# Optimization experiments

Hardware: AMD Instinct MI355X
Metric: run time of the kernel (lower is better)

## Reference

```python
import jax, jax.numpy as jnp
import numpy as np

BBOX_STD_DEV = jnp.array([0.1, 0.1, 0.2, 0.2], dtype=jnp.float32)
MIN_CONF = 0.15          # hardcoded in source (tf.where(probs >= 0.15))
NMS_THR = 0.3            # config.DETECTION_NMS_THRESHOLD
MAX_INST = 100           # config.DETECTION_MAX_INSTANCES
B, N = 8, 2048


def apply_box_deltas(boxes, deltas):
    # boxes: [N,4] (y1,x1,y2,x2); deltas: [N,4] (dy,dx,log dh,log dw)
    h = boxes[:, 2] - boxes[:, 0]
    w = boxes[:, 3] - boxes[:, 1]
    cy = boxes[:, 0] + 0.5 * h + deltas[:, 0] * h
    cx = boxes[:, 1] + 0.5 * w + deltas[:, 1] * w
    h = h * jnp.exp(deltas[:, 2])
    w = w * jnp.exp(deltas[:, 3])
    y1 = cy - 0.5 * h
    x1 = cx - 0.5 * w
    return jnp.stack([y1, x1, y1 + h, x1 + w], axis=1)


def clip_boxes(boxes, window):
    wy1, wx1, wy2, wx2 = window[0], window[1], window[2], window[3]
    y1 = jnp.clip(boxes[:, 0], wy1, wy2)
    x1 = jnp.clip(boxes[:, 1], wx1, wx2)
    y2 = jnp.clip(boxes[:, 2], wy1, wy2)
    x2 = jnp.clip(boxes[:, 3], wx1, wx2)
    return jnp.stack([y1, x1, y2, x2], axis=1)


def pairwise_iou(boxes):
    # boxes: [N,4] -> iou: [N,N]
    y1, x1, y2, x2 = boxes[:, 0], boxes[:, 1], boxes[:, 2], boxes[:, 3]
    area = (y2 - y1) * (x2 - x1)
    iy1 = jnp.maximum(y1[:, None], y1[None, :])
    ix1 = jnp.maximum(x1[:, None], x1[None, :])
    iy2 = jnp.minimum(y2[:, None], y2[None, :])
    ix2 = jnp.minimum(x2[:, None], x2[None, :])
    inter = jnp.maximum(iy2 - iy1, 0.0) * jnp.maximum(ix2 - ix1, 0.0)
    union = area[:, None] + area[None, :] - inter
    return inter / (union + 1e-8)


def refine_one(rois_i, probs_i, deltas_i, window_i):
    scores = probs_i[:, 0]
    boxes = clip_boxes(apply_box_deltas(rois_i, deltas_i * BBOX_STD_DEV), window_i)
    valid = scores >= MIN_CONF  # confidence filter (mask instead of gather)

    # sort by score descending; greedy NMS over sorted order
    order = jnp.argsort(-scores)
    sb, ss, sv = boxes[order], scores[order], valid[order]
    iou = pairwise_iou(sb)  # [N,N]
    idx = jnp.arange(N)

    def step(kept, xs):
        i, row, v = xs
        suppressed = jnp.any(kept & (idx < i) & (row > NMS_THR))
        return kept.at[i].set(v & ~suppressed), None

    kept, _ = jax.lax.scan(step, jnp.zeros((N,), dtype=bool), (idx, iou, sv))

    # top-k kept by score (already sorted desc, so top_k over masked scores)
    masked = jnp.where(kept, ss, -jnp.inf)
    _, top_i = jax.lax.top_k(masked, MAX_INST)
    ok = kept[top_i]
    det = jnp.concatenate([sb[top_i], ss[top_i][:, None]], axis=1)  # [MAX_INST,5]
    return jnp.where(ok[:, None], det, 0.0)  # zero-pad slots past num kept


def setup_inputs() -> dict:
    key = jax.random.key(0)
    k1, k2, k3 = jax.random.split(key, 3)
    # well-formed normalized rois: y1<y2, x1<x2
    yy = jnp.sort(jax.random.uniform(k1, (B, N, 2)), axis=-1)
    xx = jnp.sort(jax.random.uniform(jax.random.fold_in(k1, 1), (B, N, 2)), axis=-1)
    rois = jnp.stack([yy[..., 0], xx[..., 0], yy[..., 1], xx[..., 1]], axis=-1)
    bbox_scores = jax.random.uniform(k2, (B, N, 1), dtype=jnp.float32)
    deltas = jax.random.normal(k3, (B, N, 4), dtype=jnp.float32) * 0.1
    window = jnp.tile(jnp.array([[0.02, 0.02, 0.98, 0.98]], dtype=jnp.float32), (B, 1))
    return {"rois": rois, "bbox_scores": bbox_scores, "deltas": deltas, "window": window}


def reference(rois, bbox_scores, deltas, window):
    # -> [B, MAX_INST, 5] (y1,x1,y2,x2,score), normalized coords, zero padded
    return jax.vmap(refine_one)(rois, bbox_scores, deltas, window)
```

## Files before the change

kernel.cpp:

```cpp
#include <hip/hip_runtime.h>
#include <math.h>

#define NBOX 2048
#define NBATCH 8
#define MAX_INST 100
#define MIN_CONF 0.15f
#define NMS_THR 0.3f
#define BLOCK 512
#define NWAVE 8

typedef unsigned long long ull;

__device__ inline float4 decode_box(float4 r, float4 d,
                                    float wy1, float wx1, float wy2, float wx2) {
    float h  = __fsub_rn(r.z, r.x);
    float w  = __fsub_rn(r.w, r.y);
    float dy = __fmul_rn(d.x, 0.1f);
    float dx = __fmul_rn(d.y, 0.1f);
    float dh = __fmul_rn(d.z, 0.2f);
    float dw = __fmul_rn(d.w, 0.2f);
    float cy = __fadd_rn(__fadd_rn(r.x, __fmul_rn(0.5f, h)), __fmul_rn(dy, h));
    float cx = __fadd_rn(__fadd_rn(r.y, __fmul_rn(0.5f, w)), __fmul_rn(dx, w));
    float h2 = __fmul_rn(h, expf(dh));
    float w2 = __fmul_rn(w, expf(dw));
    float y1 = __fsub_rn(cy, __fmul_rn(0.5f, h2));
    float x1 = __fsub_rn(cx, __fmul_rn(0.5f, w2));
    float y2 = __fadd_rn(y1, h2);
    float x2 = __fadd_rn(x1, w2);
    float4 b;
    b.x = fminf(fmaxf(y1, wy1), wy2);
    b.y = fminf(fmaxf(x1, wx1), wx2);
    b.z = fminf(fmaxf(y2, wy1), wy2);
    b.w = fminf(fmaxf(x2, wx1), wx2);
    return b;
}

__device__ inline float iou_pair(float4 a, float4 b) {
    float areaA = __fmul_rn(__fsub_rn(a.z, a.x), __fsub_rn(a.w, a.y));
    float areaB = __fmul_rn(__fsub_rn(b.z, b.x), __fsub_rn(b.w, b.y));
    float iy1 = fmaxf(a.x, b.x);
    float ix1 = fmaxf(a.y, b.y);
    float iy2 = fminf(a.z, b.z);
    float ix2 = fminf(a.w, b.w);
    float ih = fmaxf(__fsub_rn(iy2, iy1), 0.0f);
    float iw = fmaxf(__fsub_rn(ix2, ix1), 0.0f);
    float inter = __fmul_rn(ih, iw);
    float uni = __fadd_rn(__fsub_rn(__fadd_rn(areaA, areaB), inter), 1e-8f);
    return __fdiv_rn(inter, uni);
}

__device__ inline ull shfl_xor64(ull x, int d) {
    unsigned lo = (unsigned)x, hi = (unsigned)(x >> 32);
    lo = __shfl_xor(lo, d);
    hi = __shfl_xor(hi, d);
    return ((ull)hi << 32) | lo;
}

__device__ inline void cmpsel(ull& a, ull& b, bool takeMinA) {
    ull mn = a < b ? a : b;
    ull mx = a < b ? b : a;
    a = takeMinA ? mn : mx;
    b = takeMinA ? mx : mn;
}

__global__ __launch_bounds__(BLOCK)
void detect_refine_kernel(const float* __restrict__ rois,
                          const float* __restrict__ scores_in,
                          const float* __restrict__ deltas,
                          const float* __restrict__ window,
                          float* __restrict__ out) {
    const int b    = blockIdx.x;
    const int tid  = threadIdx.x;
    const int lane = tid & 63;
    const int wid  = tid >> 6;

    __shared__ ull    keys[NBOX];
    __shared__ float4 sboxes[NBOX];
    __shared__ float  sscores[NBOX];
    __shared__ ull    dead8[NWAVE];
    __shared__ float4 s_keptbox[MAX_INST];
    __shared__ float  s_keptscore[MAX_INST];
    __shared__ int    s_m;

    const float wy1 = window[b * 4 + 0];
    const float wx1 = window[b * 4 + 1];
    const float wy2 = window[b * 4 + 2];
    const float wx2 = window[b * 4 + 3];

    float* outb = out + (size_t)b * MAX_INST * 5;

    for (int e = tid; e < NBOX; e += BLOCK) {
        float4 r = ((const float4*)rois)[b * NBOX + e];
        float4 d = ((const float4*)deltas)[b * NBOX + e];
        float  s = scores_in[b * NBOX + e];
        sboxes[e]  = decode_box(r, d, wy1, wx1, wy2, wx2);
        sscores[e] = s;
    }

    const int e0 = tid * 4;
    ull v[4];
    {
        float4 sc = ((const float4*)(scores_in + (size_t)b * NBOX))[tid];
        float s4[4] = {sc.x, sc.y, sc.z, sc.w};
#pragma unroll
        for (int s = 0; s < 4; ++s) {
            unsigned u = __float_as_uint(s4[s]);
            u = (u & 0x80000000u) ? ~u : (u | 0x80000000u);
            v[s] = ((ull)(~u) << 32) | (unsigned)(e0 + s);
        }
    }

    for (unsigned k = 2; k <= NBOX; k <<= 1) {
        if (k >= 512) {
#pragma unroll
            for (int s = 0; s < 4; ++s) keys[e0 + s] = v[s];
            __syncthreads();
            for (unsigned j = k >> 1; j >= 256; j >>= 1) {
                for (int t = tid; t < NBOX / 2; t += BLOCK) {
                    int i = 2 * t - (t & (j - 1));
                    int p = i | j;
                    bool up = ((i & k) == 0);
                    ull a = keys[i], c = keys[p];
                    bool sw = up ? (a > c) : (a < c);
                    if (sw) { keys[i] = c; keys[p] = a; }
                }
                __syncthreads();
            }
#pragma unroll
            for (int s = 0; s < 4; ++s) v[s] = keys[e0 + s];
        }
        unsigned jstart = ((k >> 1) > 128u) ? 128u : (k >> 1);
        for (unsigned j = jstart; j >= 4; j >>= 1) {
            int d = (int)(j >> 2);
#pragma unroll
            for (int s = 0; s < 4; ++s) {
                ull p = shfl_xor64(v[s], d);
                int e = e0 + s;
                bool takeMin = (((e & j) == 0) == ((e & k) == 0));
                v[s] = takeMin ? (v[s] < p ? v[s] : p) : (v[s] > p ? v[s] : p);
            }
        }
        if (k >= 4) {
            bool up = ((e0 & k) == 0);
            cmpsel(v[0], v[2], up);
            cmpsel(v[1], v[3], up);
        }
        {
            bool upA = ((e0 & k) == 0);
            bool upB = (((e0 + 2) & k) == 0);
            cmpsel(v[0], v[1], upA);
            cmpsel(v[2], v[3], upB);
        }
    }
#pragma unroll
    for (int s = 0; s < 4; ++s) keys[e0 + s] = v[s];
    __syncthreads();

    int count = 0;
    for (int base = 0; base < NBOX && count < MAX_INST; base += 64) {
        int    oi = (int)(keys[base + lane] & 0xFFFFFFFFull);
        float4 bj = sboxes[oi];
        float  sj = sscores[oi];

        bool deadp = (sj < MIN_CONF);
        for (int k = wid; k < count; k += NWAVE)
            deadp |= (iou_pair(s_keptbox[k], bj) > NMS_THR);
        ull bal = __ballot(deadp);
        if (lane == 0) dead8[wid] = bal;
        __syncthreads();

        if (wid == 0) {
            ull dead = dead8[0];
#pragma unroll
            for (int w2 = 1; w2 < NWAVE; ++w2) dead |= dead8[w2];
            ull alive = ~dead;
            int m = 0;
            const int maxm = MAX_INST - count;
            while (alive && m < maxm) {
                int i = __builtin_ctzll(alive);
                float4 kb;
                kb.x = __shfl(bj.x, i);
                kb.y = __shfl(bj.y, i);
                kb.z = __shfl(bj.z, i);
                kb.w = __shfl(bj.w, i);
                float ks = __shfl(sj, i);
                if (lane == 0) {
                    s_keptbox[count + m]   = kb;
                    s_keptscore[count + m] = ks;
                }
                ++m;
                ull sup = __ballot(iou_pair(kb, bj) > NMS_THR);
                alive &= ~sup;
                alive &= ~(1ull << i);
            }
            if (lane == 0) s_m = m;
        }
        __syncthreads();
        count += s_m;
    }

    for (int i = tid; i < MAX_INST * 5; i += BLOCK) {
        int r = i / 5, c = i % 5;
        float vout = 0.0f;
        if (r < count) {
            float4 bb = s_keptbox[r];
            vout = (c == 0) ? bb.x
                 : (c == 1) ? bb.y
                 : (c == 2) ? bb.z
                 : (c == 3) ? bb.w
                 :            s_keptscore[r];
        }
        outb[i] = vout;
    }
}

extern "C" void kernel_launch(void* const* d_in, const int* in_sizes, int n_in,
                              void* d_out, int out_size, void* d_ws, size_t ws_size,
                              hipStream_t stream) {
    const float* rois    = (const float*)d_in[0];
    const float* scores  = (const float*)d_in[1];
    const float* deltas  = (const float*)d_in[2];
    const float* window  = (const float*)d_in[3];
    float* out = (float*)d_out;
    detect_refine_kernel<<<NBATCH, BLOCK, 0, stream>>>(rois, scores, deltas, window, out);
}
```

Before: 47.05 us.

## Split into decode, sort and NMS kernels with 128-wide NMS chunks

```diff
diff --git a/kernel.cpp b/kernel.cpp
--- a/kernel.cpp
+++ b/kernel.cpp
@@ -6,8 +6,8 @@
 #define MAX_INST 100
 #define MIN_CONF 0.15f
 #define NMS_THR 0.3f
-#define BLOCK 512
-#define NWAVE 8
+#define SBLOCK 512
+#define NBLOCK 1024
 
 typedef unsigned long long ull;
 
@@ -63,40 +63,23 @@
     b = takeMinA ? mx : mn;
 }
 
-__global__ __launch_bounds__(BLOCK)
-void detect_refine_kernel(const float* __restrict__ rois,
-                          const float* __restrict__ scores_in,
-                          const float* __restrict__ deltas,
-                          const float* __restrict__ window,
-                          float* __restrict__ out) {
-    const int b    = blockIdx.x;
-    const int tid  = threadIdx.x;
-    const int lane = tid & 63;
-    const int wid  = tid >> 6;
-
-    __shared__ ull    keys[NBOX];
-    __shared__ float4 sboxes[NBOX];
-    __shared__ float  sscores[NBOX];
-    __shared__ ull    dead8[NWAVE];
-    __shared__ float4 s_keptbox[MAX_INST];
-    __shared__ float  s_keptscore[MAX_INST];
-    __shared__ int    s_m;
-
-    const float wy1 = window[b * 4 + 0];
-    const float wx1 = window[b * 4 + 1];
-    const float wy2 = window[b * 4 + 2];
-    const float wx2 = window[b * 4 + 3];
-
-    float* outb = out + (size_t)b * MAX_INST * 5;
-
-    for (int e = tid; e < NBOX; e += BLOCK) {
-        float4 r = ((const float4*)rois)[b * NBOX + e];
-        float4 d = ((const float4*)deltas)[b * NBOX + e];
-        float  s = scores_in[b * NBOX + e];
-        sboxes[e]  = decode_box(r, d, wy1, wx1, wy2, wx2);
-        sscores[e] = s;
-    }
-
+__global__ __launch_bounds__(256)
+void k_decode(const float* __restrict__ rois,
+              const float* __restrict__ deltas,
+              const float* __restrict__ window,
+              float4* __restrict__ wsbox) {
+    int g = blockIdx.x * 256 + threadIdx.x;
+    int b = g >> 11;
+    float4 r = ((const float4*)rois)[g];
+    float4 d = ((const float4*)deltas)[g];
+    wsbox[g] = decode_box(r, d, window[b * 4 + 0], window[b * 4 + 1],
+                          window[b * 4 + 2], window[b * 4 + 3]);
+}
+
+__global__ __launch_bounds__(SBLOCK)
+void k_sort(const float* __restrict__ scores_in, ull* __restrict__ wskeys) {
+    __shared__ ull keys[NBOX];
+    const int b = blockIdx.x, tid = threadIdx.x;
     const int e0 = tid * 4;
     ull v[4];
     {
@@ -109,14 +92,13 @@
             v[s] = ((ull)(~u) << 32) | (unsigned)(e0 + s);
         }
     }
-
     for (unsigned k = 2; k <= NBOX; k <<= 1) {
         if (k >= 512) {
 #pragma unroll
             for (int s = 0; s < 4; ++s) keys[e0 + s] = v[s];
             __syncthreads();
             for (unsigned j = k >> 1; j >= 256; j >>= 1) {
-                for (int t = tid; t < NBOX / 2; t += BLOCK) {
+                for (int t = tid; t < NBOX / 2; t += SBLOCK) {
                     int i = 2 * t - (t & (j - 1));
                     int p = i | j;
                     bool up = ((i & k) == 0);
@@ -152,65 +134,118 @@
             cmpsel(v[2], v[3], upB);
         }
     }
-#pragma unroll
-    for (int s = 0; s < 4; ++s) keys[e0 + s] = v[s];
+    ulonglong2* wk = (ulonglong2*)(wskeys + (size_t)b * NBOX);
+    ulonglong2 w0; w0.x = v[0]; w0.y = v[1];
+    ulonglong2 w1; w1.x = v[2]; w1.y = v[3];
+    wk[tid * 2]     = w0;
+    wk[tid * 2 + 1] = w1;
+}
+
+__global__ __launch_bounds__(NBLOCK)
+void k_nms(const float4* __restrict__ wsbox,
+           const ull* __restrict__ wskeys,
+           const float* __restrict__ scores_in,
+           float* __restrict__ out) {
+    const int b = blockIdx.x, tid = threadIdx.x;
+    const int lane = tid & 63, wid = tid >> 6;
+
+    __shared__ float4 sbox[NBOX];
+    __shared__ float  sscore[NBOX];
+    __shared__ ull    skeys[NBOX];
+    __shared__ ull    sdead[2][8];
+    __shared__ float4 skept[MAX_INST];
+    __shared__ float  skeptsc[MAX_INST];
+    __shared__ int    s_m;
+
+    const size_t bb = (size_t)b * NBOX;
+    for (int i = tid; i < NBOX; i += NBLOCK) {
+        sbox[i]   = wsbox[bb + i];
+        skeys[i]  = wskeys[bb + i];
+        sscore[i] = scores_in[bb + i];
+    }
     __syncthreads();
 
+    const int h  = wid & 1;
+    const int st = wid >> 1;
+
+    int oi0 = (int)(skeys[h * 64 + lane] & 0xFFFFFFFFull);
+    float4 bx = sbox[oi0];
+    float  sc = sscore[oi0];
+    float4 bxB; float scB;
+    if (wid == 0) {
+        int oiB = (int)(skeys[64 + lane] & 0xFFFFFFFFull);
+        bxB = sbox[oiB]; scB = sscore[oiB];
+    }
+
     int count = 0;
-    for (int base = 0; base < NBOX && count < MAX_INST; base += 64) {
-        int    oi = (int)(keys[base + lane] & 0xFFFFFFFFull);
-        float4 bj = sboxes[oi];
-        float  sj = sscores[oi];
-
-        bool deadp = (sj < MIN_CONF);
-        for (int k = wid; k < count; k += NWAVE)
-            deadp |= (iou_pair(s_keptbox[k], bj) > NMS_THR);
+    for (int base = 0; base < NBOX && count < MAX_INST; base += 128) {
+        float4 nbx = bx; float nsc = sc;
+        float4 nbxB = bx; float nscB = 0.f;
+        const bool havenext = (base + 128 < NBOX);
+        if (havenext) {
+            int noi = (int)(skeys[base + 128 + h * 64 + lane] & 0xFFFFFFFFull);
+            nbx = sbox[noi]; nsc = sscore[noi];
+            if (wid == 0) {
+                int noiB = (int)(skeys[base + 192 + lane] & 0xFFFFFFFFull);
+                nbxB = sbox[noiB]; nscB = sscore[noiB];
+            }
+        }
+
+        bool deadp = (sc < MIN_CONF);
+        for (int k = st; k < count; k += 8)
+            deadp |= (iou_pair(skept[k], bx) > NMS_THR);
         ull bal = __ballot(deadp);
-        if (lane == 0) dead8[wid] = bal;
+        if (lane == 0) sdead[h][st] = bal;
         __syncthreads();
 
         if (wid == 0) {
-            ull dead = dead8[0];
-#pragma unroll
-            for (int w2 = 1; w2 < NWAVE; ++w2) dead |= dead8[w2];
-            ull alive = ~dead;
+            ull d0 = sdead[0][0], d1 = sdead[1][0];
+#pragma unroll
+            for (int q = 1; q < 8; ++q) { d0 |= sdead[0][q]; d1 |= sdead[1][q]; }
+            ull a0 = ~d0, a1 = ~d1;
             int m = 0;
             const int maxm = MAX_INST - count;
-            while (alive && m < maxm) {
-                int i = __builtin_ctzll(alive);
-                float4 kb;
-                kb.x = __shfl(bj.x, i);
-                kb.y = __shfl(bj.y, i);
-                kb.z = __shfl(bj.z, i);
-                kb.w = __shfl(bj.w, i);
-                float ks = __shfl(sj, i);
-                if (lane == 0) {
-                    s_keptbox[count + m]   = kb;
-                    s_keptscore[count + m] = ks;
+            while ((a0 | a1) && m < maxm) {
+                const bool inA = (a0 != 0);
+                const int il = inA ? __builtin_ctzll(a0) : __builtin_ctzll(a1);
+                float4 kb; float ks;
+                if (inA) {
+                    kb.x = __shfl(bx.x, il); kb.y = __shfl(bx.y, il);
+                    kb.z = __shfl(bx.z, il); kb.w = __shfl(bx.w, il);
+                    ks = __shfl(sc, il);
+                } else {
+                    kb.x = __shfl(bxB.x, il); kb.y = __shfl(bxB.y, il);
+                    kb.z = __shfl(bxB.z, il); kb.w = __shfl(bxB.w, il);
+                    ks = __shfl(scB, il);
                 }
+                if (lane == 0) { skept[count + m] = kb; skeptsc[count + m] = ks; }
                 ++m;
-                ull sup = __ballot(iou_pair(kb, bj) > NMS_THR);
-                alive &= ~sup;
-                alive &= ~(1ull << i);
+                ull supA = __ballot(iou_pair(kb, bx)  > NMS_THR);
+                ull supB = __ballot(iou_pair(kb, bxB) > NMS_THR);
+                if (inA) supA |= (1ull << il); else supB |= (1ull << il);
+                a0 &= ~supA; a1 &= ~supB;
             }
             if (lane == 0) s_m = m;
         }
         __syncthreads();
         count += s_m;
-    }
-
-    for (int i = tid; i < MAX_INST * 5; i += BLOCK) {
+
+        bx = nbx; sc = nsc;
+        if (wid == 0) { bxB = nbxB; scB = nscB; }
+    }
+
+    for (int i = tid; i < MAX_INST * 5; i += NBLOCK) {
         int r = i / 5, c = i % 5;
-        float vout = 0.0f;
+        float vv = 0.0f;
         if (r < count) {
-            float4 bb = s_keptbox[r];
-            vout = (c == 0) ? bb.x
-                 : (c == 1) ? bb.y
-                 : (c == 2) ? bb.z
-                 : (c == 3) ? bb.w
-                 :            s_keptscore[r];
-        }
-        outb[i] = vout;
+            float4 kb = skept[r];
+            vv = (c == 0) ? kb.x
+               : (c == 1) ? kb.y
+               : (c == 2) ? kb.z
+               : (c == 3) ? kb.w
+               :            skeptsc[r];
+        }
+        out[(size_t)b * MAX_INST * 5 + i] = vv;
     }
 }
 
@@ -222,5 +257,11 @@
     const float* deltas  = (const float*)d_in[2];
     const float* window  = (const float*)d_in[3];
     float* out = (float*)d_out;
-    detect_refine_kernel<<<NBATCH, BLOCK, 0, stream>>>(rois, scores, deltas, window, out);
-}
+
+    float4* wsbox  = (float4*)d_ws;
+    ull*    wskeys = (ull*)((char*)d_ws + (size_t)NBATCH * NBOX * sizeof(float4));
+
+    k_decode<<<NBATCH * NBOX / 256, 256, 0, stream>>>(rois, deltas, window, wsbox);
+    k_sort<<<NBATCH, SBLOCK, 0, stream>>>(scores, wskeys);
+    k_nms<<<NBATCH, NBLOCK, 0, stream>>>(wsbox, wskeys, scores, out);
+}
```

New measurement: 65.23 us. 1.39x slower.

## Pipeline NMS windows: precompute next window's suppression while wave 0 runs greedy scan

Applied to the files above, without the earlier changes.

```diff
diff --git a/kernel.cpp b/kernel.cpp
--- a/kernel.cpp
+++ b/kernel.cpp
@@ -7,7 +7,7 @@
 #define MIN_CONF 0.15f
 #define NMS_THR 0.3f
 #define BLOCK 512
-#define NWAVE 8
+#define NWIN 16
 
 typedef unsigned long long ull;
 
@@ -35,13 +35,12 @@
     return b;
 }
 
-__device__ inline float iou_pair(float4 a, float4 b) {
-    float areaA = __fmul_rn(__fsub_rn(a.z, a.x), __fsub_rn(a.w, a.y));
-    float areaB = __fmul_rn(__fsub_rn(b.z, b.x), __fsub_rn(b.w, b.y));
-    float iy1 = fmaxf(a.x, b.x);
-    float ix1 = fmaxf(a.y, b.y);
-    float iy2 = fminf(a.z, b.z);
-    float ix2 = fminf(a.w, b.w);
+__device__ inline float iou_pa(float ax, float ay, float az, float aw2, float areaA,
+                               float4 b, float areaB) {
+    float iy1 = fmaxf(ax,  b.x);
+    float ix1 = fmaxf(ay,  b.y);
+    float iy2 = fminf(az,  b.z);
+    float ix2 = fminf(aw2, b.w);
     float ih = fmaxf(__fsub_rn(iy2, iy1), 0.0f);
     float iw = fmaxf(__fsub_rn(ix2, ix1), 0.0f);
     float inter = __fmul_rn(ih, iw);
@@ -61,6 +60,10 @@
     ull mx = a < b ? b : a;
     a = takeMinA ? mn : mx;
     b = takeMinA ? mx : mn;
+}
+
+__device__ inline float readlane_f(float x, int sl) {
+    return __uint_as_float((unsigned)__builtin_amdgcn_readlane((int)__float_as_uint(x), sl));
 }
 
 __global__ __launch_bounds__(BLOCK)
@@ -77,9 +80,10 @@
     __shared__ ull    keys[NBOX];
     __shared__ float4 sboxes[NBOX];
     __shared__ float  sscores[NBOX];
-    __shared__ ull    dead8[NWAVE];
-    __shared__ float4 s_keptbox[MAX_INST];
-    __shared__ float  s_keptscore[MAX_INST];
+    __shared__ ull    sdead[2][2][8];
+    __shared__ float4 skept[MAX_INST];
+    __shared__ float  skeptsc[MAX_INST];
+    __shared__ float  skeptar[MAX_INST];
     __shared__ int    s_m;
 
     const float wy1 = window[b * 4 + 0];
@@ -156,61 +160,114 @@
     for (int s = 0; s < 4; ++s) keys[e0 + s] = v[s];
     __syncthreads();
 
+#define LDCAND(W, B0, B1, S0, S1, A0, A1)                                   \
+    {                                                                       \
+        int base_ = (W) << 7;                                               \
+        int o0_ = (int)(keys[base_ + lane]      & 0xFFFFFFFFull);           \
+        int o1_ = (int)(keys[base_ + 64 + lane] & 0xFFFFFFFFull);           \
+        B0 = sboxes[o0_]; B1 = sboxes[o1_];                                 \
+        S0 = sscores[o0_]; S1 = sscores[o1_];                               \
+        A0 = __fmul_rn(__fsub_rn(B0.z, B0.x), __fsub_rn(B0.w, B0.y));       \
+        A1 = __fmul_rn(__fsub_rn(B1.z, B1.x), __fsub_rn(B1.w, B1.y));       \
+    }
+
+    float4 c0, c1, n0, n1;
+    float  cs0, cs1, ns0, ns1, ca0, ca1, na0, na1;
+
+    LDCAND(0, c0, c1, cs0, cs1, ca0, ca1);
+    if (wid == 0) {
+        if (lane < 2) sdead[0][lane][0] = 0;
+    } else {
+        bool d0p = (wid == 1) && (cs0 < MIN_CONF);
+        bool d1p = (wid == 1) && (cs1 < MIN_CONF);
+        ull b0 = __ballot(d0p), b1 = __ballot(d1p);
+        if (lane == 0) { sdead[0][0][wid] = b0; sdead[0][1][wid] = b1; }
+    }
+    __syncthreads();
+
     int count = 0;
-    for (int base = 0; base < NBOX && count < MAX_INST; base += 64) {
-        int    oi = (int)(keys[base + lane] & 0xFFFFFFFFull);
-        float4 bj = sboxes[oi];
-        float  sj = sscores[oi];
-
-        bool deadp = (sj < MIN_CONF);
-        for (int k = wid; k < count; k += NWAVE)
-            deadp |= (iou_pair(s_keptbox[k], bj) > NMS_THR);
-        ull bal = __ballot(deadp);
-        if (lane == 0) dead8[wid] = bal;
-        __syncthreads();
+    for (int w = 0; w < NWIN; ++w) {
+        const int par = w & 1, pnx = par ^ 1;
+        const int cnt0 = count;
 
         if (wid == 0) {
-            ull dead = dead8[0];
-#pragma unroll
-            for (int w2 = 1; w2 < NWAVE; ++w2) dead |= dead8[w2];
-            ull alive = ~dead;
+            ull d0 = 0, d1 = 0;
+#pragma unroll
+            for (int q = 0; q < 8; ++q) { d0 |= sdead[par][0][q]; d1 |= sdead[par][1][q]; }
+            ull al0 = ~d0, al1 = ~d1;
             int m = 0;
-            const int maxm = MAX_INST - count;
-            while (alive && m < maxm) {
-                int i = __builtin_ctzll(alive);
-                float4 kb;
-                kb.x = __shfl(bj.x, i);
-                kb.y = __shfl(bj.y, i);
-                kb.z = __shfl(bj.z, i);
-                kb.w = __shfl(bj.w, i);
-                float ks = __shfl(sj, i);
+            const int maxm = MAX_INST - cnt0;
+            while ((al0 | al1) && m < maxm) {
+                const bool inA = (al0 != 0);
+                ull aw = inA ? al0 : al1;
+                int il = __builtin_amdgcn_readfirstlane((int)__builtin_ctzll(aw));
+                float kx = readlane_f(inA ? c0.x : c1.x, il);
+                float ky = readlane_f(inA ? c0.y : c1.y, il);
+                float kz = readlane_f(inA ? c0.z : c1.z, il);
+                float kw = readlane_f(inA ? c0.w : c1.w, il);
+                float ka = readlane_f(inA ? ca0  : ca1,  il);
+                float ks = readlane_f(inA ? cs0  : cs1,  il);
                 if (lane == 0) {
-                    s_keptbox[count + m]   = kb;
-                    s_keptscore[count + m] = ks;
+                    skept[cnt0 + m]   = make_float4(kx, ky, kz, kw);
+                    skeptsc[cnt0 + m] = ks;
+                    skeptar[cnt0 + m] = ka;
                 }
                 ++m;
-                ull sup = __ballot(iou_pair(kb, bj) > NMS_THR);
-                alive &= ~sup;
-                alive &= ~(1ull << i);
+                ull supA = __ballot(iou_pa(kx, ky, kz, kw, ka, c0, ca0) > NMS_THR);
+                ull supB = __ballot(iou_pa(kx, ky, kz, kw, ka, c1, ca1) > NMS_THR);
+                if (inA) supA |= (1ull << il); else supB |= (1ull << il);
+                al0 &= ~supA; al1 &= ~supB;
             }
             if (lane == 0) s_m = m;
+        } else if (w + 1 < NWIN) {
+            LDCAND(w + 1, n0, n1, ns0, ns1, na0, na1);
+            bool d0p = (wid == 1) && (ns0 < MIN_CONF);
+            bool d1p = (wid == 1) && (ns1 < MIN_CONF);
+            for (int k = wid - 1; k < cnt0; k += 7) {
+                float4 kb = skept[k]; float ka = skeptar[k];
+                d0p |= (iou_pa(kb.x, kb.y, kb.z, kb.w, ka, n0, na0) > NMS_THR);
+                d1p |= (iou_pa(kb.x, kb.y, kb.z, kb.w, ka, n1, na1) > NMS_THR);
+            }
+            ull b0 = __ballot(d0p), b1 = __ballot(d1p);
+            if (lane == 0) { sdead[pnx][0][wid] = b0; sdead[pnx][1][wid] = b1; }
         }
         __syncthreads();
+
         count += s_m;
-    }
+        if (count >= MAX_INST || w + 1 >= NWIN) break;
+
+        if (wid == 0) LDCAND(w + 1, n0, n1, ns0, ns1, na0, na1);
+        {
+            bool d0i = false, d1i = false;
+            for (int k = cnt0 + wid; k < count; k += 8) {
+                float4 kb = skept[k]; float ka = skeptar[k];
+                d0i |= (iou_pa(kb.x, kb.y, kb.z, kb.w, ka, n0, na0) > NMS_THR);
+                d1i |= (iou_pa(kb.x, kb.y, kb.z, kb.w, ka, n1, na1) > NMS_THR);
+            }
+            ull b0 = __ballot(d0i), b1 = __ballot(d1i);
+            if (lane == 0) {
+                if (wid == 0) { sdead[pnx][0][0] = b0;  sdead[pnx][1][0] = b1; }
+                else          { sdead[pnx][0][wid] |= b0; sdead[pnx][1][wid] |= b1; }
+            }
+        }
+        __syncthreads();
+
+        c0 = n0; c1 = n1; cs0 = ns0; cs1 = ns1; ca0 = na0; ca1 = na1;
+    }
+#undef LDCAND
 
     for (int i = tid; i < MAX_INST * 5; i += BLOCK) {
         int r = i / 5, c = i % 5;
-        float vout = 0.0f;
+        float vv = 0.0f;
         if (r < count) {
-            float4 bb = s_keptbox[r];
-            vout = (c == 0) ? bb.x
-                 : (c == 1) ? bb.y
-                 : (c == 2) ? bb.z
-                 : (c == 3) ? bb.w
-                 :            s_keptscore[r];
-        }
-        outb[i] = vout;
+            float4 kb = skept[r];
+            vv = (c == 0) ? kb.x
+               : (c == 1) ? kb.y
+               : (c == 2) ? kb.z
+               : (c == 3) ? kb.w
+               :            skeptsc[r];
+        }
+        outb[i] = vv;
     }
 }
 
```

Result: slower. 56.86 us (+20.9%).

## Decode boxes after sort in sorted order, precompute areas, use readlane in NMS

Applied to the files above, without the earlier changes.

```diff
diff --git a/kernel.cpp b/kernel.cpp
--- a/kernel.cpp
+++ b/kernel.cpp
@@ -35,13 +35,12 @@
     return b;
 }
 
-__device__ inline float iou_pair(float4 a, float4 b) {
-    float areaA = __fmul_rn(__fsub_rn(a.z, a.x), __fsub_rn(a.w, a.y));
-    float areaB = __fmul_rn(__fsub_rn(b.z, b.x), __fsub_rn(b.w, b.y));
-    float iy1 = fmaxf(a.x, b.x);
-    float ix1 = fmaxf(a.y, b.y);
-    float iy2 = fminf(a.z, b.z);
-    float ix2 = fminf(a.w, b.w);
+__device__ inline float iou_pa(float ax, float ay, float az, float aw2, float areaA,
+                               float4 b, float areaB) {
+    float iy1 = fmaxf(ax,  b.x);
+    float ix1 = fmaxf(ay,  b.y);
+    float iy2 = fminf(az,  b.z);
+    float ix2 = fminf(aw2, b.w);
     float ih = fmaxf(__fsub_rn(iy2, iy1), 0.0f);
     float iw = fmaxf(__fsub_rn(ix2, ix1), 0.0f);
     float inter = __fmul_rn(ih, iw);
@@ -61,6 +60,10 @@
     ull mx = a < b ? b : a;
     a = takeMinA ? mn : mx;
     b = takeMinA ? mx : mn;
+}
+
+__device__ inline float readlane_f(float x, int sl) {
+    return __uint_as_float((unsigned)__builtin_amdgcn_readlane((int)__float_as_uint(x), sl));
 }
 
 __global__ __launch_bounds__(BLOCK)
@@ -75,11 +78,13 @@
     const int wid  = tid >> 6;
 
     __shared__ ull    keys[NBOX];
-    __shared__ float4 sboxes[NBOX];
-    __shared__ float  sscores[NBOX];
+    __shared__ float4 sbox[NBOX];
+    __shared__ float  sarea[NBOX];
+    __shared__ float  sscore[NBOX];
     __shared__ ull    dead8[NWAVE];
-    __shared__ float4 s_keptbox[MAX_INST];
-    __shared__ float  s_keptscore[MAX_INST];
+    __shared__ float4 skept[MAX_INST];
+    __shared__ float  skeptar[MAX_INST];
+    __shared__ float  skeptsc[MAX_INST];
     __shared__ int    s_m;
 
     const float wy1 = window[b * 4 + 0];
@@ -88,14 +93,6 @@
     const float wx2 = window[b * 4 + 3];
 
     float* outb = out + (size_t)b * MAX_INST * 5;
-
-    for (int e = tid; e < NBOX; e += BLOCK) {
-        float4 r = ((const float4*)rois)[b * NBOX + e];
-        float4 d = ((const float4*)deltas)[b * NBOX + e];
-        float  s = scores_in[b * NBOX + e];
-        sboxes[e]  = decode_box(r, d, wy1, wx1, wy2, wx2);
-        sscores[e] = s;
-    }
 
     const int e0 = tid * 4;
     ull v[4];
@@ -109,7 +106,6 @@
             v[s] = ((ull)(~u) << 32) | (unsigned)(e0 + s);
         }
     }
-
     for (unsigned k = 2; k <= NBOX; k <<= 1) {
         if (k >= 512) {
 #pragma unroll
@@ -152,19 +148,40 @@
             cmpsel(v[2], v[3], upB);
         }
     }
-#pragma unroll
-    for (int s = 0; s < 4; ++s) keys[e0 + s] = v[s];
+
+#pragma unroll
+    for (int s = 0; s < 4; ++s) {
+        int r = e0 + s;
+        int oi = (int)(v[s] & 0xFFFFFFFFull);
+        float4 rr = ((const float4*)rois)[b * NBOX + oi];
+        float4 dd = ((const float4*)deltas)[b * NBOX + oi];
+        float4 bb = decode_box(rr, dd, wy1, wx1, wy2, wx2);
+        sbox[r]   = bb;
+        sarea[r]  = __fmul_rn(__fsub_rn(bb.z, bb.x), __fsub_rn(bb.w, bb.y));
+        sscore[r] = scores_in[b * NBOX + oi];
+    }
     __syncthreads();
 
     int count = 0;
     for (int base = 0; base < NBOX && count < MAX_INST; base += 64) {
-        int    oi = (int)(keys[base + lane] & 0xFFFFFFFFull);
-        float4 bj = sboxes[oi];
-        float  sj = sscores[oi];
-
-        bool deadp = (sj < MIN_CONF);
-        for (int k = wid; k < count; k += NWAVE)
-            deadp |= (iou_pair(s_keptbox[k], bj) > NMS_THR);
+        float4 cb = sbox[base + lane];
+        float  ca = sarea[base + lane];
+        float  cs = sscore[base + lane];
+
+        bool deadp = (cs < MIN_CONF);
+        {
+            int k = wid;
+            for (; k + 8 < count; k += 16) {
+                float4 k1 = skept[k];     float a1 = skeptar[k];
+                float4 k2 = skept[k + 8]; float a2 = skeptar[k + 8];
+                deadp |= (iou_pa(k1.x, k1.y, k1.z, k1.w, a1, cb, ca) > NMS_THR);
+                deadp |= (iou_pa(k2.x, k2.y, k2.z, k2.w, a2, cb, ca) > NMS_THR);
+            }
+            if (k < count) {
+                float4 k1 = skept[k]; float a1 = skeptar[k];
+                deadp |= (iou_pa(k1.x, k1.y, k1.z, k1.w, a1, cb, ca) > NMS_THR);
+            }
+        }
         ull bal = __ballot(deadp);
         if (lane == 0) dead8[wid] = bal;
         __syncthreads();
@@ -172,26 +189,27 @@
         if (wid == 0) {
             ull dead = dead8[0];
 #pragma unroll
-            for (int w2 = 1; w2 < NWAVE; ++w2) dead |= dead8[w2];
+            for (int q = 1; q < NWAVE; ++q) dead |= dead8[q];
             ull alive = ~dead;
             int m = 0;
             const int maxm = MAX_INST - count;
             while (alive && m < maxm) {
-                int i = __builtin_ctzll(alive);
-                float4 kb;
-                kb.x = __shfl(bj.x, i);
-                kb.y = __shfl(bj.y, i);
-                kb.z = __shfl(bj.z, i);
-                kb.w = __shfl(bj.w, i);
-                float ks = __shfl(sj, i);
+                int il = __builtin_amdgcn_readfirstlane((int)__builtin_ctzll(alive));
+                float kx = readlane_f(cb.x, il);
+                float ky = readlane_f(cb.y, il);
+                float kz = readlane_f(cb.z, il);
+                float kw = readlane_f(cb.w, il);
+                float ka = readlane_f(ca,   il);
+                float ks = readlane_f(cs,   il);
                 if (lane == 0) {
-                    s_keptbox[count + m]   = kb;
-                    s_keptscore[count + m] = ks;
+                    skept[count + m]   = make_float4(kx, ky, kz, kw);
+                    skeptar[count + m] = ka;
+                    skeptsc[count + m] = ks;
                 }
                 ++m;
-                ull sup = __ballot(iou_pair(kb, bj) > NMS_THR);
+                ull sup = __ballot(iou_pa(kx, ky, kz, kw, ka, cb, ca) > NMS_THR);
                 alive &= ~sup;
-                alive &= ~(1ull << i);
+                alive &= ~(1ull << il);
             }
             if (lane == 0) s_m = m;
         }
@@ -201,16 +219,16 @@
 
     for (int i = tid; i < MAX_INST * 5; i += BLOCK) {
         int r = i / 5, c = i % 5;
-        float vout = 0.0f;
+        float vv = 0.0f;
         if (r < count) {
-            float4 bb = s_keptbox[r];
-            vout = (c == 0) ? bb.x
-                 : (c == 1) ? bb.y
-                 : (c == 2) ? bb.z
-                 : (c == 3) ? bb.w
-                 :            s_keptscore[r];
-        }
-        outb[i] = vout;
+            float4 kb = skept[r];
+            vv = (c == 0) ? kb.x
+               : (c == 1) ? kb.y
+               : (c == 2) ? kb.z
+               : (c == 3) ? kb.w
+               :            skeptsc[r];
+        }
+        outb[i] = vv;
     }
 }
 
```

Measured after the change: 49.44 us. 5.1% more time.
